# Kernel optimization log

Measured on AMD Instinct MI355X. Metric: run time of the kernel, lower is better.

## Reference

```python
import jax, jax.numpy as jnp
import numpy as np

N_USERS = 50000
N_ENTITIES = 100000
CHANNEL = 64
N_FACTORS = 4
N_REL = 9  # n_relations; weight has N_REL-1 rows
N_EDGES = 1_500_000
NNZ = 800_000
N_HOPS = 2


def _l2_normalize(x, eps=1e-12):
    # matches torch F.normalize(dim=1)
    n = jnp.sqrt(jnp.sum(x * x, axis=1, keepdims=True))
    return x / jnp.maximum(n, eps)


def _distance_correlation(t1, t2):
    # t1, t2: [d] rows of disen_weight_att (d = n_relations-1)
    ch = t1.shape[0]
    t1 = t1[:, None]
    t2 = t2[:, None]
    a_ = (t1 @ t1.T) * 2.0
    b_ = (t2 @ t2.T) * 2.0
    t1s = t1 ** 2
    t2s = t2 ** 2
    a = jnp.sqrt(jnp.maximum(t1s - a_ + t1s.T, 0.0) + 1e-8)
    b = jnp.sqrt(jnp.maximum(t2s - b_ + t2s.T, 0.0) + 1e-8)
    A = a - a.mean(axis=0, keepdims=True) - a.mean(axis=1, keepdims=True) + a.mean()
    B = b - b.mean(axis=0, keepdims=True) - b.mean(axis=1, keepdims=True) + b.mean()
    dcov_AB = jnp.sqrt(jnp.maximum((A * B).sum() / ch ** 2, 0.0) + 1e-8)
    dcov_AA = jnp.sqrt(jnp.maximum((A * A).sum() / ch ** 2, 0.0) + 1e-8)
    dcov_BB = jnp.sqrt(jnp.maximum((B * B).sum() / ch ** 2, 0.0) + 1e-8)
    return dcov_AB / jnp.sqrt(dcov_AA * dcov_BB + 1e-8)


def _cul_cor(disen_weight_att):
    cor = jnp.asarray(0.0, disen_weight_att.dtype)
    for i in range(N_FACTORS):
        for j in range(i + 1, N_FACTORS):
            cor = cor + _distance_correlation(disen_weight_att[i], disen_weight_att[j])
    return cor


def setup_inputs() -> dict:
    key = jax.random.key(0)
    ks = jax.random.split(key, 11)
    return {
        "user_emb": jax.random.normal(ks[0], (N_USERS, CHANNEL), jnp.float32) * 0.1,
        "entity_emb": jax.random.normal(ks[1], (N_ENTITIES, CHANNEL), jnp.float32) * 0.1,
        "latent_emb": jax.random.normal(ks[2], (N_FACTORS, CHANNEL), jnp.float32) * 0.1,
        "weight": jax.random.normal(ks[3], (N_REL - 1, CHANNEL), jnp.float32) * 0.1,
        "disen_weight_att": jax.random.normal(ks[4], (N_FACTORS, N_REL - 1), jnp.float32) * 0.1,
        "interact_vals": jax.random.uniform(ks[5], (NNZ,), jnp.float32),
        "head": jax.random.randint(ks[6], (N_EDGES,), 0, N_ENTITIES),
        "tail": jax.random.randint(ks[7], (N_EDGES,), 0, N_ENTITIES),
        "edge_type": jax.random.randint(ks[8], (N_EDGES,), 1, N_REL),  # in [1, N_REL-1]
        "interact_rows": jax.random.randint(ks[9], (NNZ,), 0, N_USERS),
        "interact_cols": jax.random.randint(ks[10], (NNZ,), 0, N_ENTITIES),
    }


def reference(user_emb, entity_emb, latent_emb, weight, disen_weight_att,
              interact_vals, head, tail, edge_type, interact_rows, interact_cols):
    n_entities = entity_emb.shape[0]
    n_users = user_emb.shape[0]
    cor = _cul_cor(disen_weight_att)

    entity_res = entity_emb
    user_res = user_emb
    ones_e = jnp.ones((head.shape[0],), entity_emb.dtype)
    cnt = jax.ops.segment_sum(ones_e, head, num_segments=n_entities)  # reused: head fixed
    cnt = jnp.maximum(cnt, 1.0)[:, None]

    for _ in range(N_HOPS):
        # KG aggregate: gather tail emb * relation emb, scatter-mean by head
        rel_emb = weight[edge_type - 1]                      # [E, C]
        msg = entity_emb[tail] * rel_emb                     # [E, C]
        entity_agg = jax.ops.segment_sum(msg, head, num_segments=n_entities) / cnt

        # user -> latent factor attention
        score = jax.nn.softmax(user_emb @ latent_emb.T, axis=1)   # [U, F]

        # user aggregate: sparse.mm(interact_mat, entity_emb)
        gathered = interact_vals[:, None] * entity_emb[interact_cols]  # [nnz, C]
        user_agg = jax.ops.segment_sum(gathered, interact_rows, num_segments=n_users)

        disen_weight = jax.nn.softmax(disen_weight_att, axis=-1) @ weight  # [F, C]
        mix = score @ disen_weight                                          # [U, C]
        user_new = user_agg * mix + user_agg

        entity_emb = _l2_normalize(entity_agg)
        user_emb = _l2_normalize(user_new)
        entity_res = entity_res + entity_emb
        user_res = user_res + user_emb

    return entity_res, user_res, cor
```

## Files before the change

kernel.cpp:

```cpp
#include <hip/hip_runtime.h>
#include <math.h>

constexpr int CH         = 64;
constexpr int N_USERS    = 50000;
constexpr int N_ENTITIES = 100000;
constexpr int N_FACTORS  = 4;
constexpr int N_RELM1    = 8;
constexpr int N_EDGES    = 1500000;
constexpr int NNZ        = 800000;

constexpr int NBE        = (N_ENTITIES + 255) / 256;
constexpr int NBU        = (N_USERS + 255) / 256;
constexpr int NBKT       = NBE + NBU;
constexpr int TOTAL      = N_EDGES + NNZ;
constexpr int IPB        = 8192;
constexpr int NBLK       = (TOTAL + IPB - 1) / IPB;
constexpr int ENT_BLK8   = N_ENTITIES / 8;
constexpr int USR_BLK8   = N_USERS / 8;

typedef unsigned int u32;
typedef float __attribute__((ext_vector_type(4))) f32x4;
typedef unsigned int __attribute__((ext_vector_type(4))) u32x4;

__device__ __forceinline__ u32 pack_bf16x2(float a, float b) {
    u32 ua = __float_as_uint(a), ub = __float_as_uint(b);
    u32 ra = (ua + 0x7FFFu + ((ua >> 16) & 1u)) >> 16;
    u32 rb = (ub + 0x7FFFu + ((ub >> 16) & 1u)) >> 16;
    return ra | (rb << 16);
}
__device__ __forceinline__ float bf_lo(u32 v) { return __uint_as_float(v << 16); }
__device__ __forceinline__ float bf_hi(u32 v) { return __uint_as_float(v & 0xFFFF0000u); }

__device__ __forceinline__ float4 nt_ld4f(const float4* p) {
    f32x4 v = __builtin_nontemporal_load((const f32x4*)p);
    return make_float4(v.x, v.y, v.z, v.w);
}
__device__ __forceinline__ void nt_st4f(float4* p, float4 v) {
    f32x4 t; t.x = v.x; t.y = v.y; t.z = v.z; t.w = v.w;
    __builtin_nontemporal_store(t, (f32x4*)p);
}
__device__ __forceinline__ void nt_st4u(uint4* p, uint4 v) {
    u32x4 t; t.x = v.x; t.y = v.y; t.z = v.z; t.w = v.w;
    __builtin_nontemporal_store(t, (u32x4*)p);
}
__device__ __forceinline__ int   nt_ldi(const int* p)   { return __builtin_nontemporal_load(p); }
__device__ __forceinline__ float nt_ldf(const float* p) { return __builtin_nontemporal_load(p); }

__device__ __forceinline__ uint4 gz(const u32* __restrict__ t, int r, int c8, bool v) {
    uint4 x = make_uint4(0u, 0u, 0u, 0u);
    if (v) x = ((const uint4*)t)[r * 8 + c8];
    return x;
}

__device__ __forceinline__ int coarse_bucket(int i, const int* __restrict__ head,
                                             const int* __restrict__ irows) {
    return (i < N_EDGES) ? (head[i] >> 8) : (NBE + (irows[i - N_EDGES] >> 8));
}

__global__ __launch_bounds__(256)
void count_coarse(const int* __restrict__ head, const int* __restrict__ irows,
                  int* __restrict__ H) {
    __shared__ int hist[NBKT];
    for (int j = threadIdx.x; j < NBKT; j += 256) hist[j] = 0;
    __syncthreads();
    int start = blockIdx.x * IPB;
    int end   = min(start + IPB, TOTAL);
    for (int i = start + threadIdx.x; i < end; i += 256)
        atomicAdd(&hist[coarse_bucket(i, head, irows)], 1);
    __syncthreads();
    for (int j = threadIdx.x; j < NBKT; j += 256)
        H[j * NBLK + blockIdx.x] = hist[j];
}

__global__ __launch_bounds__(64)
void scan_hcols(int* __restrict__ H, int* __restrict__ T) {
    int b = blockIdx.x, lane = threadIdx.x;
    int carry = 0;
    #pragma unroll
    for (int c = 0; c < (NBLK + 63) / 64; ++c) {
        int idx = c * 64 + lane;
        int v = (idx < NBLK) ? H[b * NBLK + idx] : 0;
        int incl = v;
        #pragma unroll
        for (int d = 1; d < 64; d <<= 1) {
            int u = __shfl_up(incl, d, 64);
            if (lane >= d) incl += u;
        }
        if (idx < NBLK) H[b * NBLK + idx] = carry + incl - v;
        carry += __shfl(incl, 63, 64);
    }
    if (lane == 0) T[b] = carry;
}

__global__ __launch_bounds__(1024)
void scan_buckets(const int* __restrict__ T, int* __restrict__ Bb) {
    __shared__ int lds[1024];
    int t = threadIdx.x;
    int v = (t < NBKT) ? T[t] : 0;
    lds[t] = v;
    __syncthreads();
    for (int d = 1; d < 1024; d <<= 1) {
        int u = (t >= d) ? lds[t - d] : 0;
        __syncthreads();
        lds[t] += u;
        __syncthreads();
    }
    if (t < NBKT) Bb[t] = lds[t] - v;
    if (t == NBKT - 1) Bb[NBKT] = lds[t];
}

__global__ __launch_bounds__(256)
void scatter_stage(const int* __restrict__ head, const int* __restrict__ tail,
                   const int* __restrict__ etype,
                   const int* __restrict__ irows, const int* __restrict__ icols,
                   const float* __restrict__ ivals,
                   const int* __restrict__ H, const int* __restrict__ Bb,
                   int2* __restrict__ stageE, int2* __restrict__ stageU,
                   float* __restrict__ stageUv) {
    __shared__ int cur[NBKT];
    for (int j = threadIdx.x; j < NBKT; j += 256)
        cur[j] = Bb[j] + H[j * NBLK + blockIdx.x];
    __syncthreads();
    int start = blockIdx.x * IPB;
    int end   = min(start + IPB, TOTAL);
    for (int i = start + threadIdx.x; i < end; i += 256) {
        if (i < N_EDGES) {
            int k   = head[i];
            int pay = tail[i] | ((etype[i] - 1) << 20);
            int pos = atomicAdd(&cur[k >> 8], 1);
            stageE[pos] = make_int2(k, pay);
        } else {
            int ii  = i - N_EDGES;
            int k   = irows[ii];
            int pos = atomicAdd(&cur[NBE + (k >> 8)], 1) - N_EDGES;
            stageU[pos]  = make_int2(k, icols[ii]);
            stageUv[pos] = ivals[ii];
        }
    }
}

__global__ __launch_bounds__(256)
void bin_fill(const int* __restrict__ Bb,
              const int2* __restrict__ stageE, const int2* __restrict__ stageU,
              const float* __restrict__ stageUv,
              int* __restrict__ offE, int* __restrict__ offU,
              int* __restrict__ elst, int* __restrict__ ucol,
              float* __restrict__ uval) {
    __shared__ int khist[256];
    __shared__ int cur[256];
    int b = blockIdx.x, t = threadIdx.x;
    khist[t] = 0;
    __syncthreads();
    if (b < NBE) {
        int lo = Bb[b], hi = Bb[b + 1];
        for (int i = lo + t; i < hi; i += 256)
            atomicAdd(&khist[stageE[i].x & 255], 1);
        __syncthreads();
        int v = khist[t];
        for (int d = 1; d < 256; d <<= 1) {
            int u = (t >= d) ? khist[t - d] : 0;
            __syncthreads();
            khist[t] += u;
            __syncthreads();
        }
        int excl = lo + khist[t] - v;
        int key  = b * 256 + t;
        if (key < N_ENTITIES) offE[key] = excl;
        cur[t] = excl;
        __syncthreads();
        for (int i = lo + t; i < hi; i += 256) {
            int2 s = stageE[i];
            int p = atomicAdd(&cur[s.x & 255], 1);
            elst[p] = s.y;
        }
        if (b == 0 && t == 0) offE[N_ENTITIES] = N_EDGES;
    } else {
        int lo = Bb[b] - N_EDGES, hi = Bb[b + 1] - N_EDGES;
        for (int i = lo + t; i < hi; i += 256)
            atomicAdd(&khist[stageU[i].x & 255], 1);
        __syncthreads();
        int v = khist[t];
        for (int d = 1; d < 256; d <<= 1) {
            int u = (t >= d) ? khist[t - d] : 0;
            __syncthreads();
            khist[t] += u;
            __syncthreads();
        }
        int excl = lo + khist[t] - v;
        int key  = (b - NBE) * 256 + t;
        if (key < N_USERS) offU[key] = excl;
        cur[t] = excl;
        __syncthreads();
        for (int i = lo + t; i < hi; i += 256) {
            int2 s = stageU[i];
            float vv = stageUv[i];
            int p = atomicAdd(&cur[s.x & 255], 1);
            ucol[p] = s.y;
            uval[p] = vv;
        }
        if (b == NBE && t == 0) offU[N_USERS] = NNZ;
    }
}

__global__ __launch_bounds__(256)
void to_bf16(const float* __restrict__ src, u32* __restrict__ dst, int n2) {
    int i = blockIdx.x * 256 + threadIdx.x;
    if (i < n2) {
        float2 f = ((const float2*)src)[i];
        dst[i] = pack_bf16x2(f.x, f.y);
    }
}

__device__ __forceinline__ void acc_edge(float* acc, uint4 xv, float4 wa, float4 wb) {
    acc[0] += bf_lo(xv.x) * wa.x; acc[1] += bf_hi(xv.x) * wa.y;
    acc[2] += bf_lo(xv.y) * wa.z; acc[3] += bf_hi(xv.y) * wa.w;
    acc[4] += bf_lo(xv.z) * wb.x; acc[5] += bf_hi(xv.z) * wb.y;
    acc[6] += bf_lo(xv.w) * wb.z; acc[7] += bf_hi(xv.w) * wb.w;
}
__device__ __forceinline__ void acc_user(float* acc, uint4 xv, float vv) {
    acc[0] += vv * bf_lo(xv.x); acc[1] += vv * bf_hi(xv.x);
    acc[2] += vv * bf_lo(xv.y); acc[3] += vv * bf_hi(xv.y);
    acc[4] += vv * bf_lo(xv.z); acc[5] += vv * bf_hi(xv.z);
    acc[6] += vv * bf_lo(xv.w); acc[7] += vv * bf_hi(xv.w);
}

template <bool HOP0>
__global__ __launch_bounds__(256)
void hop_pass(const u32* __restrict__ entB,
              const float* __restrict__ usr_in,
              const float* __restrict__ weight, const float* __restrict__ latent,
              const float* __restrict__ dw,
              const int* __restrict__ offE, const int* __restrict__ elst,
              const int* __restrict__ offU, const int* __restrict__ ucol,
              const float* __restrict__ uval,
              u32* __restrict__ AeB_out,
              float* __restrict__ Au_out,
              float* __restrict__ ent_res, float* __restrict__ usr_res,
              const float* __restrict__ ent_base, const float* __restrict__ usr_base) {
    __shared__ float4 w4[N_RELM1 * 16];
    int lane = threadIdx.x & 63;
    int h    = lane >> 5;
    int g    = (lane >> 3) & 3;
    int c8   = lane & 7;
    int l5   = lane & 31;
    float acc[8] = {0.f, 0.f, 0.f, 0.f, 0.f, 0.f, 0.f, 0.f};

    if ((int)blockIdx.x < ENT_BLK8) {
        if (threadIdx.x < N_RELM1 * 16)
            w4[threadIdx.x] = ((const float4*)weight)[threadIdx.x];
        __syncthreads();
        int row = blockIdx.x * 8 + ((threadIdx.x >> 6) << 1) + h;
        int lo = offE[row], hi = offE[row + 1];
        for (int k0 = lo; k0 < hi; k0 += 32) {
            int m = min(32, hi - k0);
            int p = nt_ldi(&elst[min(k0 + l5, N_EDGES - 1)]);
            for (int jj = 0; jj < m; jj += 16) {
                int j0 = jj + g;
                int q0 = __shfl(p, j0,      32);
                int q1 = __shfl(p, j0 + 4,  32);
                int q2 = __shfl(p, j0 + 8,  32);
                int q3 = __shfl(p, j0 + 12, 32);
                uint4 x0 = gz(entB, q0 & 0xFFFFF, c8, j0      < m);
                uint4 x1 = gz(entB, q1 & 0xFFFFF, c8, j0 + 4  < m);
                uint4 x2 = gz(entB, q2 & 0xFFFFF, c8, j0 + 8  < m);
                uint4 x3 = gz(entB, q3 & 0xFFFFF, c8, j0 + 12 < m);
                float4 wa0 = w4[(q0 >> 20) * 16 + (c8 << 1)];
                float4 wb0 = w4[(q0 >> 20) * 16 + (c8 << 1) + 1];
                float4 wa1 = w4[(q1 >> 20) * 16 + (c8 << 1)];
                float4 wb1 = w4[(q1 >> 20) * 16 + (c8 << 1) + 1];
                float4 wa2 = w4[(q2 >> 20) * 16 + (c8 << 1)];
                float4 wb2 = w4[(q2 >> 20) * 16 + (c8 << 1) + 1];
                float4 wa3 = w4[(q3 >> 20) * 16 + (c8 << 1)];
                float4 wb3 = w4[(q3 >> 20) * 16 + (c8 << 1) + 1];
                acc_edge(acc, x0, wa0, wb0);
                acc_edge(acc, x1, wa1, wb1);
                acc_edge(acc, x2, wa2, wb2);
                acc_edge(acc, x3, wa3, wb3);
            }
        }
        #pragma unroll
        for (int j = 0; j < 8; ++j) {
            acc[j] += __shfl_xor(acc[j], 8, 64);
            acc[j] += __shfl_xor(acc[j], 16, 64);
        }
        float s = 0.0f;
        #pragma unroll
        for (int j = 0; j < 8; ++j) s += acc[j] * acc[j];
        s += __shfl_xor(s, 1, 64);
        s += __shfl_xor(s, 2, 64);
        s += __shfl_xor(s, 4, 64);
        float inv = 1.0f / fmaxf(sqrtf(s), 1e-12f);
        if (g == 0) {
            float y0 = acc[0] * inv, y1 = acc[1] * inv, y2 = acc[2] * inv, y3 = acc[3] * inv;
            float y4 = acc[4] * inv, y5 = acc[5] * inv, y6 = acc[6] * inv, y7 = acc[7] * inv;
            int qi = row * 16 + (c8 << 1);
            if (HOP0) {
                uint4 pk;
                pk.x = pack_bf16x2(y0, y1); pk.y = pack_bf16x2(y2, y3);
                pk.z = pack_bf16x2(y4, y5); pk.w = pack_bf16x2(y6, y7);
                nt_st4u(&((uint4*)AeB_out)[row * 8 + c8], pk);
                float4 b0 = nt_ld4f(&((const float4*)ent_base)[qi]);
                float4 b1 = nt_ld4f(&((const float4*)ent_base)[qi + 1]);
                nt_st4f(&((float4*)ent_res)[qi],     make_float4(b0.x + y0, b0.y + y1, b0.z + y2, b0.w + y3));
                nt_st4f(&((float4*)ent_res)[qi + 1], make_float4(b1.x + y4, b1.y + y5, b1.z + y6, b1.w + y7));
            } else {
                float4 r0 = nt_ld4f(&((const float4*)ent_res)[qi]);
                float4 r1 = nt_ld4f(&((const float4*)ent_res)[qi + 1]);
                nt_st4f(&((float4*)ent_res)[qi],     make_float4(r0.x + y0, r0.y + y1, r0.z + y2, r0.w + y3));
                nt_st4f(&((float4*)ent_res)[qi + 1], make_float4(r1.x + y4, r1.y + y5, r1.z + y6, r1.w + y7));
            }
        }
    } else {
        int row = (blockIdx.x - ENT_BLK8) * 8 + ((threadIdx.x >> 6) << 1) + h;
        int qi  = row * 16 + (c8 << 1);
        float4 u0 = nt_ld4f(&((const float4*)usr_in)[qi]);
        float4 u1 = nt_ld4f(&((const float4*)usr_in)[qi + 1]);
        int lo = offU[row], hi = offU[row + 1];
        for (int k0 = lo; k0 < hi; k0 += 32) {
            int m = min(32, hi - k0);
            int sidx = min(k0 + l5, NNZ - 1);
            int   cl = nt_ldi(&ucol[sidx]);
            float vl = nt_ldf(&uval[sidx]);
            for (int jj = 0; jj < m; jj += 16) {
                int j0 = jj + g;
                int   c0 = __shfl(cl, j0,      32);
                int   c1 = __shfl(cl, j0 + 4,  32);
                int   c2 = __shfl(cl, j0 + 8,  32);
                int   c3 = __shfl(cl, j0 + 12, 32);
                float v0 = __shfl(vl, j0,      32);
                float v1 = __shfl(vl, j0 + 4,  32);
                float v2 = __shfl(vl, j0 + 8,  32);
                float v3 = __shfl(vl, j0 + 12, 32);
                uint4 x0 = gz(entB, c0, c8, j0      < m);
                uint4 x1 = gz(entB, c1, c8, j0 + 4  < m);
                uint4 x2 = gz(entB, c2, c8, j0 + 8  < m);
                uint4 x3 = gz(entB, c3, c8, j0 + 12 < m);
                acc_user(acc, x0, v0);
                acc_user(acc, x1, v1);
                acc_user(acc, x2, v2);
                acc_user(acc, x3, v3);
            }
        }
        #pragma unroll
        for (int j = 0; j < 8; ++j) {
            acc[j] += __shfl_xor(acc[j], 8, 64);
            acc[j] += __shfl_xor(acc[j], 16, 64);
        }
        float d[N_FACTORS];
        #pragma unroll
        for (int f = 0; f < N_FACTORS; ++f) {
            float4 l0 = ((const float4*)latent)[f * 16 + (c8 << 1)];
            float4 l1 = ((const float4*)latent)[f * 16 + (c8 << 1) + 1];
            d[f] = u0.x * l0.x + u0.y * l0.y + u0.z * l0.z + u0.w * l0.w
                 + u1.x * l1.x + u1.y * l1.y + u1.z * l1.z + u1.w * l1.w;
            d[f] += __shfl_xor(d[f], 1, 64);
            d[f] += __shfl_xor(d[f], 2, 64);
            d[f] += __shfl_xor(d[f], 4, 64);
        }
        float mx = fmaxf(fmaxf(d[0], d[1]), fmaxf(d[2], d[3]));
        float ex0 = expf(d[0] - mx), ex1 = expf(d[1] - mx);
        float ex2 = expf(d[2] - mx), ex3 = expf(d[3] - mx);
        float sinv = 1.0f / (ex0 + ex1 + ex2 + ex3);
        float mix[8] = {0.f, 0.f, 0.f, 0.f, 0.f, 0.f, 0.f, 0.f};
        {
            float exf[N_FACTORS] = {ex0, ex1, ex2, ex3};
            #pragma unroll
            for (int f = 0; f < N_FACTORS; ++f) {
                float4 w0 = ((const float4*)dw)[f * 16 + (c8 << 1)];
                float4 w1 = ((const float4*)dw)[f * 16 + (c8 << 1) + 1];
                float ef = exf[f];
                mix[0] += ef * w0.x; mix[1] += ef * w0.y;
                mix[2] += ef * w0.z; mix[3] += ef * w0.w;
                mix[4] += ef * w1.x; mix[5] += ef * w1.y;
                mix[6] += ef * w1.z; mix[7] += ef * w1.w;
            }
            #pragma unroll
            for (int j = 0; j < 8; ++j) mix[j] *= sinv;
        }
        float un[8];
        #pragma unroll
        for (int j = 0; j < 8; ++j) un[j] = acc[j] * (1.0f + mix[j]);
        float s = 0.0f;
        #pragma unroll
        for (int j = 0; j < 8; ++j) s += un[j] * un[j];
        s += __shfl_xor(s, 1, 64);
        s += __shfl_xor(s, 2, 64);
        s += __shfl_xor(s, 4, 64);
        float inv = 1.0f / fmaxf(sqrtf(s), 1e-12f);
        if (g == 0) {
            float y0 = un[0] * inv, y1 = un[1] * inv, y2 = un[2] * inv, y3 = un[3] * inv;
            float y4 = un[4] * inv, y5 = un[5] * inv, y6 = un[6] * inv, y7 = un[7] * inv;
            if (HOP0) {
                nt_st4f(&((float4*)Au_out)[qi],     make_float4(y0, y1, y2, y3));
                nt_st4f(&((float4*)Au_out)[qi + 1], make_float4(y4, y5, y6, y7));
            } else {
                float4 b0 = nt_ld4f(&((const float4*)usr_base)[qi]);
                float4 b1 = nt_ld4f(&((const float4*)usr_base)[qi + 1]);
                nt_st4f(&((float4*)usr_res)[qi],
                        make_float4((b0.x + u0.x) + y0, (b0.y + u0.y) + y1,
                                    (b0.z + u0.z) + y2, (b0.w + u0.w) + y3));
                nt_st4f(&((float4*)usr_res)[qi + 1],
                        make_float4((b1.x + u1.x) + y4, (b1.y + u1.y) + y5,
                                    (b1.z + u1.z) + y6, (b1.w + u1.w) + y7));
            }
        }
    }
}

__global__ __launch_bounds__(384)
void discor_kernel(const float* __restrict__ att,
                   const float* __restrict__ weight,
                   float* __restrict__ dw,
                   float* __restrict__ cor_out) {
    __shared__ float part[6];
    if (blockIdx.x == 0) {
        if (threadIdx.x < 256) {
            int f = threadIdx.x >> 6;
            int c = threadIdx.x & 63;
            float m = -1e30f;
            #pragma unroll
            for (int j = 0; j < N_RELM1; ++j) m = fmaxf(m, att[f * N_RELM1 + j]);
            float s = 0.0f, w[N_RELM1];
            #pragma unroll
            for (int j = 0; j < N_RELM1; ++j) { w[j] = expf(att[f * N_RELM1 + j] - m); s += w[j]; }
            float acc = 0.0f;
            #pragma unroll
            for (int j = 0; j < N_RELM1; ++j) acc += w[j] * weight[j * CH + c];
            dw[f * CH + c] = acc / s;
        }
    } else {
        int w    = threadIdx.x >> 6;
        int lane = threadIdx.x & 63;
        const int pi[6] = {0, 0, 0, 1, 1, 2};
        const int pj[6] = {1, 2, 3, 2, 3, 3};
        int r = lane >> 3, c = lane & 7;
        const float* t1 = att + pi[w] * N_RELM1;
        const float* t2 = att + pj[w] * N_RELM1;
        float a  = sqrtf(fmaxf(t1[r] * t1[r] - 2.0f * t1[r] * t1[c] + t1[c] * t1[c], 0.0f) + 1e-8f);
        float bb = sqrtf(fmaxf(t2[r] * t2[r] - 2.0f * t2[r] * t2[c] + t2[c] * t2[c], 0.0f) + 1e-8f);
        float rsA = a, rsB = bb;
        #pragma unroll
        for (int o = 1; o < 8; o <<= 1) { rsA += __shfl_xor(rsA, o, 64); rsB += __shfl_xor(rsB, o, 64); }
        float csA = a, csB = bb;
        #pragma unroll
        for (int o = 8; o < 64; o <<= 1) { csA += __shfl_xor(csA, o, 64); csB += __shfl_xor(csB, o, 64); }
        float totA = rsA, totB = rsB;
        #pragma unroll
        for (int o = 8; o < 64; o <<= 1) { totA += __shfl_xor(totA, o, 64); totB += __shfl_xor(totB, o, 64); }
        float A = a  - csA * 0.125f - rsA * 0.125f + totA * (1.0f / 64.0f);
        float B = bb - csB * 0.125f - rsB * 0.125f + totB * (1.0f / 64.0f);
        float sAB = A * B, sAA = A * A, sBB = B * B;
        #pragma unroll
        for (int o = 1; o < 64; o <<= 1) {
            sAB += __shfl_xor(sAB, o, 64);
            sAA += __shfl_xor(sAA, o, 64);
            sBB += __shfl_xor(sBB, o, 64);
        }
        if (lane == 0) {
            float dAB = sqrtf(fmaxf(sAB * (1.0f / 64.0f), 0.0f) + 1e-8f);
            float dAA = sqrtf(fmaxf(sAA * (1.0f / 64.0f), 0.0f) + 1e-8f);
            float dBB = sqrtf(fmaxf(sBB * (1.0f / 64.0f), 0.0f) + 1e-8f);
            part[w] = dAB / sqrtf(dAA * dBB + 1e-8f);
        }
        __syncthreads();
        if (threadIdx.x == 0) {
            float s = 0.0f;
            for (int q = 0; q < 6; ++q) s += part[q];
            cor_out[0] = s;
        }
    }
}

extern "C" void kernel_launch(void* const* d_in, const int* in_sizes, int n_in,
                              void* d_out, int out_size, void* d_ws, size_t ws_size,
                              hipStream_t stream) {
    const float* user_emb   = (const float*)d_in[0];
    const float* entity_emb = (const float*)d_in[1];
    const float* latent     = (const float*)d_in[2];
    const float* weight     = (const float*)d_in[3];
    const float* att        = (const float*)d_in[4];
    const float* ivals      = (const float*)d_in[5];
    const int*   head       = (const int*)d_in[6];
    const int*   tail       = (const int*)d_in[7];
    const int*   etype      = (const int*)d_in[8];
    const int*   irows      = (const int*)d_in[9];
    const int*   icols      = (const int*)d_in[10];

    float* out     = (float*)d_out;
    float* ent_res = out;
    float* usr_res = out + (size_t)N_ENTITIES * CH;
    float* cor_out = out + (size_t)N_ENTITIES * CH + (size_t)N_USERS * CH;

    const size_t ENT_ELEMS = (size_t)N_ENTITIES * CH;
    const size_t USR_ELEMS = (size_t)N_USERS * CH;
    const int    ENT_PAIRS = (int)(ENT_ELEMS / 2);

    float* ws   = (float*)d_ws;
    u32*   entB = (u32*)ws;
    u32*   AeB  = entB + ENT_PAIRS;
    float* Au   = (float*)(AeB + ENT_PAIRS);
    float* dw   = Au + USR_ELEMS;
    int*   offE = (int*)(dw + N_FACTORS * CH);
    int*   offU = offE + N_ENTITIES + 1;
    int*   elst = offU + N_USERS + 1;
    int*   ucol = elst + N_EDGES;
    float* uval = (float*)(ucol + NNZ);
    int*   H    = (int*)(uval + NNZ);
    int*   T    = H + NBKT * NBLK;
    int*   Bb   = T + NBKT;
    int2*  stageE  = (int2*)entB;
    int2*  stageU  = ((int2*)entB) + N_EDGES;
    float* stageUv = (float*)(stageU + NNZ);

    discor_kernel<<<2, 384, 0, stream>>>(att, weight, dw, cor_out);

    count_coarse<<<NBLK, 256, 0, stream>>>(head, irows, H);
    scan_hcols<<<NBKT, 64, 0, stream>>>(H, T);
    scan_buckets<<<1, 1024, 0, stream>>>(T, Bb);
    scatter_stage<<<NBLK, 256, 0, stream>>>(head, tail, etype, irows, icols, ivals,
                                            H, Bb, stageE, stageU, stageUv);
    bin_fill<<<NBKT, 256, 0, stream>>>(Bb, stageE, stageU, stageUv,
                                       offE, offU, elst, ucol, uval);

    to_bf16<<<(ENT_PAIRS + 255) / 256, 256, 0, stream>>>(entity_emb, entB, ENT_PAIRS);

    hop_pass<true><<<ENT_BLK8 + USR_BLK8, 256, 0, stream>>>(
        entB, user_emb, weight, latent, dw,
        offE, elst, offU, ucol, uval,
        AeB, Au, ent_res, usr_res, entity_emb, user_emb);

    hop_pass<false><<<ENT_BLK8 + USR_BLK8, 256, 0, stream>>>(
        AeB, Au, weight, latent, dw,
        offE, elst, offU, ucol, uval,
        nullptr, nullptr, ent_res, usr_res, entity_emb, user_emb);
}
```

Measured before the change: 361.4 us.

## Pack staging records into 32-bit words and shrink CSR build block size

Result: faster. 347.9 us (-3.8%).

```diff
diff --git a/kernel.cpp b/kernel.cpp
--- a/kernel.cpp
+++ b/kernel.cpp
@@ -13,7 +13,7 @@
 constexpr int NBU        = (N_USERS + 255) / 256;
 constexpr int NBKT       = NBE + NBU;
 constexpr int TOTAL      = N_EDGES + NNZ;
-constexpr int IPB        = 8192;
+constexpr int IPB        = 2048;
 constexpr int NBLK       = (TOTAL + IPB - 1) / IPB;
 constexpr int ENT_BLK8   = N_ENTITIES / 8;
 constexpr int USR_BLK8   = N_USERS / 8;
@@ -38,10 +38,6 @@
 __device__ __forceinline__ void nt_st4f(float4* p, float4 v) {
     f32x4 t; t.x = v.x; t.y = v.y; t.z = v.z; t.w = v.w;
     __builtin_nontemporal_store(t, (f32x4*)p);
-}
-__device__ __forceinline__ void nt_st4u(uint4* p, uint4 v) {
-    u32x4 t; t.x = v.x; t.y = v.y; t.z = v.z; t.w = v.w;
-    __builtin_nontemporal_store(t, (u32x4*)p);
 }
 __device__ __forceinline__ int   nt_ldi(const int* p)   { return __builtin_nontemporal_load(p); }
 __device__ __forceinline__ float nt_ldf(const float* p) { return __builtin_nontemporal_load(p); }
@@ -76,7 +72,6 @@
 void scan_hcols(int* __restrict__ H, int* __restrict__ T) {
     int b = blockIdx.x, lane = threadIdx.x;
     int carry = 0;
-    #pragma unroll
     for (int c = 0; c < (NBLK + 63) / 64; ++c) {
         int idx = c * 64 + lane;
         int v = (idx < NBLK) ? H[b * NBLK + idx] : 0;
@@ -115,7 +110,7 @@
                    const int* __restrict__ irows, const int* __restrict__ icols,
                    const float* __restrict__ ivals,
                    const int* __restrict__ H, const int* __restrict__ Bb,
-                   int2* __restrict__ stageE, int2* __restrict__ stageU,
+                   u32* __restrict__ stageE, u32* __restrict__ stageU,
                    float* __restrict__ stageUv) {
     __shared__ int cur[NBKT];
     for (int j = threadIdx.x; j < NBKT; j += 256)
@@ -126,14 +121,14 @@
     for (int i = start + threadIdx.x; i < end; i += 256) {
         if (i < N_EDGES) {
             int k   = head[i];
-            int pay = tail[i] | ((etype[i] - 1) << 20);
+            u32 rec = (u32)tail[i] | ((u32)(etype[i] - 1) << 17) | ((u32)(k & 255) << 20);
             int pos = atomicAdd(&cur[k >> 8], 1);
-            stageE[pos] = make_int2(k, pay);
+            stageE[pos] = rec;
         } else {
             int ii  = i - N_EDGES;
             int k   = irows[ii];
             int pos = atomicAdd(&cur[NBE + (k >> 8)], 1) - N_EDGES;
-            stageU[pos]  = make_int2(k, icols[ii]);
+            stageU[pos]  = (u32)icols[ii] | ((u32)(k & 255) << 17);
             stageUv[pos] = ivals[ii];
         }
     }
@@ -141,7 +136,7 @@
 
 __global__ __launch_bounds__(256)
 void bin_fill(const int* __restrict__ Bb,
-              const int2* __restrict__ stageE, const int2* __restrict__ stageU,
+              const u32* __restrict__ stageE, const u32* __restrict__ stageU,
               const float* __restrict__ stageUv,
               int* __restrict__ offE, int* __restrict__ offU,
               int* __restrict__ elst, int* __restrict__ ucol,
@@ -154,7 +149,7 @@
     if (b < NBE) {
         int lo = Bb[b], hi = Bb[b + 1];
         for (int i = lo + t; i < hi; i += 256)
-            atomicAdd(&khist[stageE[i].x & 255], 1);
+            atomicAdd(&khist[(stageE[i] >> 20) & 255], 1);
         __syncthreads();
         int v = khist[t];
         for (int d = 1; d < 256; d <<= 1) {
@@ -169,15 +164,15 @@
         cur[t] = excl;
         __syncthreads();
         for (int i = lo + t; i < hi; i += 256) {
-            int2 s = stageE[i];
-            int p = atomicAdd(&cur[s.x & 255], 1);
-            elst[p] = s.y;
+            u32 s = stageE[i];
+            int p = atomicAdd(&cur[(s >> 20) & 255], 1);
+            elst[p] = (int)(s & 0xFFFFFu);
         }
         if (b == 0 && t == 0) offE[N_ENTITIES] = N_EDGES;
     } else {
         int lo = Bb[b] - N_EDGES, hi = Bb[b + 1] - N_EDGES;
         for (int i = lo + t; i < hi; i += 256)
-            atomicAdd(&khist[stageU[i].x & 255], 1);
+            atomicAdd(&khist[(stageU[i] >> 17) & 255], 1);
         __syncthreads();
         int v = khist[t];
         for (int d = 1; d < 256; d <<= 1) {
@@ -192,10 +187,10 @@
         cur[t] = excl;
         __syncthreads();
         for (int i = lo + t; i < hi; i += 256) {
-            int2 s = stageU[i];
+            u32 s = stageU[i];
             float vv = stageUv[i];
-            int p = atomicAdd(&cur[s.x & 255], 1);
-            ucol[p] = s.y;
+            int p = atomicAdd(&cur[(s >> 17) & 255], 1);
+            ucol[p] = (int)(s & 0x1FFFFu);
             uval[p] = vv;
         }
         if (b == NBE && t == 0) offU[N_USERS] = NNZ;
@@ -260,18 +255,18 @@
                 int q1 = __shfl(p, j0 + 4,  32);
                 int q2 = __shfl(p, j0 + 8,  32);
                 int q3 = __shfl(p, j0 + 12, 32);
-                uint4 x0 = gz(entB, q0 & 0xFFFFF, c8, j0      < m);
-                uint4 x1 = gz(entB, q1 & 0xFFFFF, c8, j0 + 4  < m);
-                uint4 x2 = gz(entB, q2 & 0xFFFFF, c8, j0 + 8  < m);
-                uint4 x3 = gz(entB, q3 & 0xFFFFF, c8, j0 + 12 < m);
-                float4 wa0 = w4[(q0 >> 20) * 16 + (c8 << 1)];
-                float4 wb0 = w4[(q0 >> 20) * 16 + (c8 << 1) + 1];
-                float4 wa1 = w4[(q1 >> 20) * 16 + (c8 << 1)];
-                float4 wb1 = w4[(q1 >> 20) * 16 + (c8 << 1) + 1];
-                float4 wa2 = w4[(q2 >> 20) * 16 + (c8 << 1)];
-                float4 wb2 = w4[(q2 >> 20) * 16 + (c8 << 1) + 1];
-                float4 wa3 = w4[(q3 >> 20) * 16 + (c8 << 1)];
-                float4 wb3 = w4[(q3 >> 20) * 16 + (c8 << 1) + 1];
+                uint4 x0 = gz(entB, q0 & 0x1FFFF, c8, j0      < m);
+                uint4 x1 = gz(entB, q1 & 0x1FFFF, c8, j0 + 4  < m);
+                uint4 x2 = gz(entB, q2 & 0x1FFFF, c8, j0 + 8  < m);
+                uint4 x3 = gz(entB, q3 & 0x1FFFF, c8, j0 + 12 < m);
+                float4 wa0 = w4[(q0 >> 17) * 16 + (c8 << 1)];
+                float4 wb0 = w4[(q0 >> 17) * 16 + (c8 << 1) + 1];
+                float4 wa1 = w4[(q1 >> 17) * 16 + (c8 << 1)];
+                float4 wb1 = w4[(q1 >> 17) * 16 + (c8 << 1) + 1];
+                float4 wa2 = w4[(q2 >> 17) * 16 + (c8 << 1)];
+                float4 wb2 = w4[(q2 >> 17) * 16 + (c8 << 1) + 1];
+                float4 wa3 = w4[(q3 >> 17) * 16 + (c8 << 1)];
+                float4 wb3 = w4[(q3 >> 17) * 16 + (c8 << 1) + 1];
                 acc_edge(acc, x0, wa0, wb0);
                 acc_edge(acc, x1, wa1, wb1);
                 acc_edge(acc, x2, wa2, wb2);
@@ -298,7 +293,7 @@
                 uint4 pk;
                 pk.x = pack_bf16x2(y0, y1); pk.y = pack_bf16x2(y2, y3);
                 pk.z = pack_bf16x2(y4, y5); pk.w = pack_bf16x2(y6, y7);
-                nt_st4u(&((uint4*)AeB_out)[row * 8 + c8], pk);
+                ((uint4*)AeB_out)[row * 8 + c8] = pk;
                 float4 b0 = nt_ld4f(&((const float4*)ent_base)[qi]);
                 float4 b1 = nt_ld4f(&((const float4*)ent_base)[qi + 1]);
                 nt_st4f(&((float4*)ent_res)[qi],     make_float4(b0.x + y0, b0.y + y1, b0.z + y2, b0.w + y3));
@@ -505,11 +500,11 @@
     int*   elst = offU + N_USERS + 1;
     int*   ucol = elst + N_EDGES;
     float* uval = (float*)(ucol + NNZ);
-    int*   H    = (int*)(uval + NNZ);
+    int*   H    = (int*)Au;
     int*   T    = H + NBKT * NBLK;
     int*   Bb   = T + NBKT;
-    int2*  stageE  = (int2*)entB;
-    int2*  stageU  = ((int2*)entB) + N_EDGES;
+    u32*   stageE  = entB;
+    u32*   stageU  = entB + N_EDGES;
     float* stageUv = (float*)(stageU + NNZ);
 
     discor_kernel<<<2, 384, 0, stream>>>(att, weight, dw, cor_out);
```
